# Optimization experiments

Hardware: AMD Instinct MI355X
Metric: run time of the kernel (lower is better)

The kernel has to match this reference:

```python
import jax, jax.numpy as jnp
import numpy as np

# Scalar-only irreps: 8x0e nodes in, 4x0e edge in, 8x0e edge out, 16x0e node out.
N = 50000          # nodes
E = 800000         # edges
MUL_NODE_IN = 8
MUL_EDGE_IN = 4
MUL_Z = 2 * MUL_NODE_IN          # cat([x[i], x[j]]) -> 16
MUL_EDGE_OUT = 8
MUL_NODE_OUT = 16
W_NUMEL = MUL_EDGE_IN * MUL_Z * MUL_EDGE_OUT  # 512 = edge_tp.weight_numel
RAD_IN, RAD_HID = 16, 64         # radial_neurons=[16, 64]


def setup_inputs() -> dict:
    key = jax.random.key(0)
    ks = jax.random.split(key, 7)
    x = jax.random.normal(ks[0], (N, MUL_NODE_IN), dtype=jnp.float32)
    edge_index = jax.random.randint(ks[1], (2, E), 0, N)
    edge_attr = jax.random.normal(ks[2], (E, MUL_EDGE_IN), dtype=jnp.float32)
    edge_len_emb = jax.random.normal(ks[3], (E, RAD_IN), dtype=jnp.float32)
    # radial MLP (e3nn FullyConnectedNet: normalized linear layers, silu)
    w1 = jax.random.normal(ks[4], (RAD_IN, RAD_HID), dtype=jnp.float32)
    w2 = jax.random.normal(ks[5], (RAD_HID, W_NUMEL), dtype=jnp.float32)
    # node_tp internal shared weights: [mul_node_in, mul_edge_out, mul_node_out]
    w_node = jax.random.normal(ks[6], (MUL_NODE_IN, MUL_EDGE_OUT, MUL_NODE_OUT), dtype=jnp.float32)
    return {"x": x, "edge_index": edge_index, "edge_attr": edge_attr,
            "edge_len_emb": edge_len_emb, "w1": w1, "w2": w2, "w_node": w_node}


def reference(x, edge_index, edge_attr, edge_len_emb, w1, w2, w_node):
    i, j = edge_index[0], edge_index[1]
    # radial MLP -> per-edge TP weights (e3nn normalized linears, silu)
    h = jax.nn.silu(edge_len_emb @ w1 / jnp.sqrt(jnp.float32(RAD_IN)))
    w_edge = (h @ w2 / jnp.sqrt(jnp.float32(RAD_HID)))
    w_edge = w_edge.reshape(E, MUL_EDGE_IN, MUL_Z, MUL_EDGE_OUT)
    # gather + concat: z = cat([x[i], x[j]])  [E, 16]
    z = jnp.concatenate([x[i], x[j]], axis=-1)
    # edge_tp: fully-connected scalar TP with path norm 1/sqrt(mul1*mul2)
    edge_out = jnp.einsum('ea,eb,eabk->ek', edge_attr, z, w_edge)
    edge_out = edge_out / jnp.sqrt(jnp.float32(MUL_EDGE_IN * MUL_Z))
    # scatter-sum to destination nodes j
    e_sum = jax.ops.segment_sum(edge_out, j, num_segments=x.shape[0])
    # node_tp: shared internal weights, path norm 1/sqrt(mul1*mul2)
    x_out = jnp.einsum('na,nb,abk->nk', x, e_sum, w_node)
    x_out = x_out / jnp.sqrt(jnp.float32(MUL_NODE_IN * MUL_EDGE_OUT))
    return (x_out, edge_out)
```

## Files before the change

### kernel.cpp

```cpp
#include <hip/hip_runtime.h>


typedef __attribute__((ext_vector_type(8))) short short8;
typedef __attribute__((ext_vector_type(4))) float floatx4;

__device__ inline unsigned short f2bf(float f) {
    union { float f; unsigned u; } v; v.f = f;
    unsigned r = v.u + 0x7FFFu + ((v.u >> 16) & 1u);
    return (unsigned short)(r >> 16);
}

__device__ inline unsigned cvt_pk_bf16(float lo, float hi) {
    unsigned r;
    asm("v_cvt_pk_bf16_f32 %0, %1, %2" : "=v"(r) : "v"(lo), "v"(hi));
    return r;
}

constexpr int TB   = 512;
constexpr int NBLK = 512;

__global__ __launch_bounds__(TB, 2) void edge_kernel(
    const float* __restrict__ x,
    const int*   __restrict__ ei,
    const float* __restrict__ attr,
    const float* __restrict__ emb,
    const float* __restrict__ w1,
    const float* __restrict__ w2,
    float* __restrict__ edge_out,
    float* __restrict__ e_sum,
    int E)
{
    __shared__ __align__(16) unsigned short s_w2t[512 * 64];
    __shared__ __align__(16) float          s_ztA[8 * 16 * 32];

    const int tid  = threadIdx.x;
    const int wave = tid >> 6;
    const int lane = tid & 63;
    const int m16  = lane & 15;
    const int quad = lane >> 4;
    const int par  = m16 >> 3;

    for (int idx = tid; idx < 512 * 64; idx += TB) {
        const int n = idx & 511, k = idx >> 9;
        s_w2t[n * 64 + (k ^ ((n & 7) << 3))] = f2bf(w2[k * 512 + n]);
    }
    __syncthreads();

    short8 w1f[4];
    #pragma unroll
    for (int mt = 0; mt < 4; ++mt) {
        short8 f;
        if (quad < 2) {
            #pragma unroll
            for (int j = 0; j < 8; ++j)
                f[j] = (short)f2bf(w1[(quad * 8 + j) * 64 + mt * 16 + m16]);
        } else {
            #pragma unroll
            for (int j = 0; j < 8; ++j) f[j] = 0;
        }
        w1f[mt] = f;
    }

    float* ztw = s_ztA + wave * 16 * 32;

    const int  wid = blockIdx.x * 8 + wave;
    const int  nw  = NBLK * 8;
    const int  ntiles = E >> 5;
    const bool stg = (quad < 2);
    const int  mst = quad * 16 + m16;

    const int srcA = m16 + 16 * ((2 * quad) & 3);
    const int srcB = m16 + 16 * ((2 * quad + 1) & 3);

    const int swz = (m16 & 7) << 3;
    const int o0  = (quad * 8) ^ swz;
    const int o1  = o0 ^ 32;

    float4 xi0, xi1, xj0, xj1, a4;
    float4 em0a, em0b, em1a, em1b;
    int viN = 0, vjN = 0, vjC = 0;

    if (wid < ntiles && stg) {
        const int e0 = (wid << 5) + mst;
        const int vi = ei[e0];
        vjC = ei[E + e0];
        xi0 = *(const float4*)(x + (size_t)vi * 8);
        xi1 = *(const float4*)(x + (size_t)vi * 8 + 4);
        xj0 = *(const float4*)(x + (size_t)vjC * 8);
        xj1 = *(const float4*)(x + (size_t)vjC * 8 + 4);
        a4  = *(const float4*)(attr + (size_t)e0 * 4);
        const float* ep0 = emb + (size_t)((wid << 5) + m16) * 16 + quad * 8;
        em0a = *(const float4*)ep0;
        em0b = *(const float4*)(ep0 + 4);
        const float* ep1 = emb + (size_t)((wid << 5) + 16 + m16) * 16 + quad * 8;
        em1a = *(const float4*)ep1;
        em1b = *(const float4*)(ep1 + 4);
        const int t1 = (wid + nw < ntiles) ? (wid + nw) : wid;
        const int e1 = (t1 << 5) + mst;
        viN = ei[e1];
        vjN = ei[E + e1];
    }

    for (int tile = wid; tile < ntiles; tile += nw) {
        const int base = tile << 5;

        if (stg) {
            ztw[ 0*32+mst]=xi0.x; ztw[ 1*32+mst]=xi0.y;
            ztw[ 2*32+mst]=xi0.z; ztw[ 3*32+mst]=xi0.w;
            ztw[ 4*32+mst]=xi1.x; ztw[ 5*32+mst]=xi1.y;
            ztw[ 6*32+mst]=xi1.z; ztw[ 7*32+mst]=xi1.w;
            ztw[ 8*32+mst]=xj0.x; ztw[ 9*32+mst]=xj0.y;
            ztw[10*32+mst]=xj0.z; ztw[11*32+mst]=xj0.w;
            ztw[12*32+mst]=xj1.x; ztw[13*32+mst]=xj1.y;
            ztw[14*32+mst]=xj1.z; ztw[15*32+mst]=xj1.w;
        }
        const float4 a4cur = a4;
        const int    vjE   = vjC;

        short8 a1[2];
        {
            union { short8 s8; unsigned u[4]; } uu;
            if (stg) {
                uu.u[0] = cvt_pk_bf16(em0a.x, em0a.y);
                uu.u[1] = cvt_pk_bf16(em0a.z, em0a.w);
                uu.u[2] = cvt_pk_bf16(em0b.x, em0b.y);
                uu.u[3] = cvt_pk_bf16(em0b.z, em0b.w);
            } else {
                uu.u[0]=0u; uu.u[1]=0u; uu.u[2]=0u; uu.u[3]=0u;
            }
            a1[0] = uu.s8;
            if (stg) {
                uu.u[0] = cvt_pk_bf16(em1a.x, em1a.y);
                uu.u[1] = cvt_pk_bf16(em1a.z, em1a.w);
                uu.u[2] = cvt_pk_bf16(em1b.x, em1b.y);
                uu.u[3] = cvt_pk_bf16(em1b.z, em1b.w);
            } else {
                uu.u[0]=0u; uu.u[1]=0u; uu.u[2]=0u; uu.u[3]=0u;
            }
            a1[1] = uu.s8;
        }

        {
            const int tn     = tile + nw;
            const int tn_cl  = (tn  < ntiles) ? tn  : tile;
            const int tnn    = tn + nw;
            const int tnn_cl = (tnn < ntiles) ? tnn : tn_cl;
            if (stg) {
                const int en = (tn_cl << 5) + mst;
                vjC = vjN;
                xi0 = *(const float4*)(x + (size_t)viN * 8);
                xi1 = *(const float4*)(x + (size_t)viN * 8 + 4);
                xj0 = *(const float4*)(x + (size_t)vjN * 8);
                xj1 = *(const float4*)(x + (size_t)vjN * 8 + 4);
                a4  = *(const float4*)(attr + (size_t)en * 4);
                const float* ep0 = emb + (size_t)((tn_cl << 5) + m16) * 16 + quad * 8;
                em0a = *(const float4*)ep0;
                em0b = *(const float4*)(ep0 + 4);
                const float* ep1 = emb + (size_t)((tn_cl << 5) + 16 + m16) * 16 + quad * 8;
                em1a = *(const float4*)ep1;
                em1b = *(const float4*)(ep1 + 4);
                const int enn = (tnn_cl << 5) + mst;
                viN = ei[enn];
                vjN = ei[E + enn];
            }
        }

        short8 a2[2][2];
        #pragma unroll
        for (int s = 0; s < 2; ++s) {
            unsigned p[4][2];
            #pragma unroll
            for (int half = 0; half < 2; ++half) {
                floatx4 c0, c1;
                {
                    floatx4 z4 = {0.f, 0.f, 0.f, 0.f};
                    c0 = __builtin_amdgcn_mfma_f32_16x16x32_bf16(w1f[2*half    ], a1[s], z4, 0, 0, 0);
                    c1 = __builtin_amdgcn_mfma_f32_16x16x32_bf16(w1f[2*half + 1], a1[s], z4, 0, 0, 0);
                }
                #pragma unroll
                for (int h = 0; h < 2; ++h) {
                    const floatx4& c = h ? c1 : c0;
                    float sv[4];
                    #pragma unroll
                    for (int r = 0; r < 4; ++r) {
                        const float u   = c[r] * 0.25f;
                        const float den = 1.f + __expf(-u);
                        sv[r] = u * __builtin_amdgcn_rcpf(den) * 0.015625f;
                    }
                    p[2*half + h][0] = cvt_pk_bf16(sv[0], sv[1]);
                    p[2*half + h][1] = cvt_pk_bf16(sv[2], sv[3]);
                }
            }
            #pragma unroll
            for (int qq = 0; qq < 2; ++qq) {
                union { short8 s8; unsigned u[4]; } uu;
                #pragma unroll
                for (int w = 0; w < 4; ++w) {
                    const int srcLane = (w < 2) ? srcA : srcB;
                    const unsigned vA = (unsigned)__shfl((int)p[2*qq    ][w & 1], srcLane, 64);
                    const unsigned vB = (unsigned)__shfl((int)p[2*qq + 1][w & 1], srcLane, 64);
                    uu.u[w] = (quad & 2) ? vB : vA;
                }
                a2[s][qq] = uu.s8;
            }
        }

        float eacc[2][4];
        #pragma unroll
        for (int s = 0; s < 2; ++s)
            #pragma unroll
            for (int r = 0; r < 4; ++r) eacc[s][r] = 0.f;

        __builtin_amdgcn_s_setprio(1);
        #pragma unroll 1
        for (int g = 0; g < 4; ++g) {
            const float ag = (g == 0) ? a4cur.x : (g == 1) ? a4cur.y
                           : (g == 2) ? a4cur.z : a4cur.w;
            float av[2][4];
            #pragma unroll
            for (int s = 0; s < 2; ++s)
                #pragma unroll
                for (int r = 0; r < 4; ++r)
                    av[s][r] = __shfl(ag, s * 16 + quad * 4 + r, 64);

            float tacc[2][4];
            #pragma unroll
            for (int s = 0; s < 2; ++s)
                #pragma unroll
                for (int r = 0; r < 4; ++r) tacc[s][r] = 0.f;

            #pragma unroll
            for (int tt = 0; tt < 8; ++tt) {
                const int t = g * 8 + tt;
                const unsigned short* wrow = s_w2t + (16 * t + m16) * 64;
                short8 b2[2];
                b2[0] = *(const short8*)(wrow + o0);
                b2[1] = *(const short8*)(wrow + o1);
                const int b_idx = (2 * tt + par) & 15;
                #pragma unroll
                for (int s = 0; s < 2; ++s) {
                    floatx4 c = {0.f, 0.f, 0.f, 0.f};
                    c = __builtin_amdgcn_mfma_f32_16x16x32_bf16(a2[s][0], b2[0], c, 0, 0, 0);
                    c = __builtin_amdgcn_mfma_f32_16x16x32_bf16(a2[s][1], b2[1], c, 0, 0, 0);
                    const float4 zv = *(const float4*)(ztw + b_idx * 32 + s * 16 + quad * 4);
                    tacc[s][0] = fmaf(c[0], zv.x, tacc[s][0]);
                    tacc[s][1] = fmaf(c[1], zv.y, tacc[s][1]);
                    tacc[s][2] = fmaf(c[2], zv.z, tacc[s][2]);
                    tacc[s][3] = fmaf(c[3], zv.w, tacc[s][3]);
                }
            }
            #pragma unroll
            for (int s = 0; s < 2; ++s)
                #pragma unroll
                for (int r = 0; r < 4; ++r)
                    eacc[s][r] = fmaf(av[s][r], tacc[s][r], eacc[s][r]);
        }
        __builtin_amdgcn_s_setprio(0);

        #pragma unroll
        for (int s = 0; s < 2; ++s)
            #pragma unroll
            for (int r = 0; r < 4; ++r)
                eacc[s][r] += __shfl_xor(eacc[s][r], 8, 64);

        int vjr[2][4];
        #pragma unroll
        for (int s = 0; s < 2; ++s)
            #pragma unroll
            for (int r = 0; r < 4; ++r)
                vjr[s][r] = __shfl(vjE, s * 16 + quad * 4 + r, 64);

        if (m16 < 8) {
            #pragma unroll
            for (int s = 0; s < 2; ++s) {
                #pragma unroll
                for (int r = 0; r < 4; ++r) {
                    const int e = base + s * 16 + quad * 4 + r;
                    edge_out[(size_t)e * 8 + m16] = eacc[s][r];
                    atomicAdd(e_sum + (size_t)vjr[s][r] * 8 + m16, eacc[s][r]);
                }
            }
        }
    }
}

__global__ __launch_bounds__(256) void node_kernel(
    const float* __restrict__ x,
    const float* __restrict__ e_sum,
    const float* __restrict__ w_node,
    float* __restrict__ x_out,
    int N)
{
    __shared__ float s_w[8 * 8 * 16];
    for (int idx = threadIdx.x; idx < 1024; idx += 256) s_w[idx] = w_node[idx];
    __syncthreads();

    const int n = blockIdx.x * 256 + threadIdx.x;
    if (n >= N) return;

    float xa[8], eb[8];
    #pragma unroll
    for (int a = 0; a < 8; ++a) xa[a] = x[(size_t)n * 8 + a];
    #pragma unroll
    for (int b = 0; b < 8; ++b) eb[b] = e_sum[(size_t)n * 8 + b];

    float out[16];
    #pragma unroll
    for (int k = 0; k < 16; ++k) out[k] = 0.f;

    const float4* wv = (const float4*)s_w;
    #pragma unroll
    for (int a = 0; a < 8; ++a) {
        #pragma unroll
        for (int b = 0; b < 8; ++b) {
            const float t = xa[a] * eb[b] * 0.125f;
            #pragma unroll
            for (int k4 = 0; k4 < 4; ++k4) {
                const float4 w = wv[(a * 8 + b) * 4 + k4];
                out[k4 * 4 + 0] = fmaf(t, w.x, out[k4 * 4 + 0]);
                out[k4 * 4 + 1] = fmaf(t, w.y, out[k4 * 4 + 1]);
                out[k4 * 4 + 2] = fmaf(t, w.z, out[k4 * 4 + 2]);
                out[k4 * 4 + 3] = fmaf(t, w.w, out[k4 * 4 + 3]);
            }
        }
    }

    float4* xo = (float4*)(x_out + (size_t)n * 16);
    #pragma unroll
    for (int k4 = 0; k4 < 4; ++k4)
        xo[k4] = make_float4(out[k4 * 4 + 0], out[k4 * 4 + 1],
                             out[k4 * 4 + 2], out[k4 * 4 + 3]);
}

extern "C" void kernel_launch(void* const* d_in, const int* in_sizes, int n_in,
                              void* d_out, int out_size, void* d_ws, size_t ws_size,
                              hipStream_t stream) {
    const float* x      = (const float*)d_in[0];
    const int*   ei     = (const int*)d_in[1];
    const float* attr   = (const float*)d_in[2];
    const float* emb    = (const float*)d_in[3];
    const float* w1     = (const float*)d_in[4];
    const float* w2     = (const float*)d_in[5];
    const float* w_node = (const float*)d_in[6];

    const int N = in_sizes[0] / 8;
    const int E = in_sizes[2] / 4;

    float* x_out    = (float*)d_out;
    float* edge_out = (float*)d_out + (size_t)N * 16;
    float* e_sum    = (float*)d_ws;

    hipMemsetAsync(e_sum, 0, (size_t)N * 8 * sizeof(float), stream);

    edge_kernel<<<NBLK, TB, 0, stream>>>(x, ei, attr, emb, w1, w2,
                                         edge_out, e_sum, E);

    node_kernel<<<(N + 255) / 256, 256, 0, stream>>>(x, e_sum, w_node, x_out, N);
}
```

Measured before the change: 205.7 us.

## Use 1024-thread blocks and stage edge attrs and dst indices in LDS

Doubles the block size to 1024 threads with half as many blocks, so one copy of the 64 KB bf16 w2 table in LDS serves 16 waves instead of 8. It also replaces the per-group cross-lane shuffles of edge attributes and destination indices with writes to per-wave LDS buffers that are read back as float4 and int4. This trades shuffle work and repeated w2 staging for extra LDS traffic and a larger LDS footprint, and launch bounds of 1024 may cap registers per thread and cause spills.

```diff
diff --git a/kernel.cpp b/kernel.cpp
--- a/kernel.cpp
+++ b/kernel.cpp
@@ -16,10 +16,13 @@
     return r;
 }
 
-constexpr int TB   = 512;
-constexpr int NBLK = 512;
-
-__global__ __launch_bounds__(TB, 2) void edge_kernel(
+constexpr int TB    = 1024;
+constexpr int NBLK  = 256;
+constexpr int NWAVE = TB / 64;
+
+constexpr int AT_LDF = 32;
+
+__global__ __launch_bounds__(TB) void edge_kernel(
     const float* __restrict__ x,
     const int*   __restrict__ ei,
     const float* __restrict__ attr,
@@ -31,7 +34,9 @@
     int E)
 {
     __shared__ __align__(16) unsigned short s_w2t[512 * 64];
-    __shared__ __align__(16) float          s_ztA[8 * 16 * 32];
+    __shared__ __align__(16) float          s_ztA[NWAVE * 16 * 32];
+    __shared__ __align__(16) float          s_atA[NWAVE * 4 * AT_LDF];
+    __shared__ int                          s_vjA[NWAVE * 32];
 
     const int tid  = threadIdx.x;
     const int wave = tid >> 6;
@@ -62,9 +67,11 @@
     }
 
     float* ztw = s_ztA + wave * 16 * 32;
-
-    const int  wid = blockIdx.x * 8 + wave;
-    const int  nw  = NBLK * 8;
+    float* atw = s_atA + wave * 4 * AT_LDF;
+    int*   vjw = s_vjA + wave * 32;
+
+    const int  wid = blockIdx.x * NWAVE + wave;
+    const int  nw  = NBLK * NWAVE;
     const int  ntiles = E >> 5;
     const bool stg = (quad < 2);
     const int  mst = quad * 16 + m16;
@@ -113,9 +120,10 @@
             ztw[10*32+mst]=xj0.z; ztw[11*32+mst]=xj0.w;
             ztw[12*32+mst]=xj1.x; ztw[13*32+mst]=xj1.y;
             ztw[14*32+mst]=xj1.z; ztw[15*32+mst]=xj1.w;
-        }
-        const float4 a4cur = a4;
-        const int    vjE   = vjC;
+            atw[0*AT_LDF+mst]=a4.x;   atw[1*AT_LDF+mst]=a4.y;
+            atw[2*AT_LDF+mst]=a4.z;   atw[3*AT_LDF+mst]=a4.w;
+            vjw[mst] = vjC;
+        }
 
         short8 a1[2];
         {
@@ -214,14 +222,13 @@
         __builtin_amdgcn_s_setprio(1);
         #pragma unroll 1
         for (int g = 0; g < 4; ++g) {
-            const float ag = (g == 0) ? a4cur.x : (g == 1) ? a4cur.y
-                           : (g == 2) ? a4cur.z : a4cur.w;
             float av[2][4];
             #pragma unroll
-            for (int s = 0; s < 2; ++s)
-                #pragma unroll
-                for (int r = 0; r < 4; ++r)
-                    av[s][r] = __shfl(ag, s * 16 + quad * 4 + r, 64);
+            for (int s = 0; s < 2; ++s) {
+                const float4 a4v = *(const float4*)(atw + g * AT_LDF + s * 16 + quad * 4);
+                av[s][0] = a4v.x; av[s][1] = a4v.y;
+                av[s][2] = a4v.z; av[s][3] = a4v.w;
+            }
 
             float tacc[2][4];
             #pragma unroll
@@ -263,21 +270,16 @@
             for (int r = 0; r < 4; ++r)
                 eacc[s][r] += __shfl_xor(eacc[s][r], 8, 64);
 
-        int vjr[2][4];
-        #pragma unroll
-        for (int s = 0; s < 2; ++s)
-            #pragma unroll
-            for (int r = 0; r < 4; ++r)
-                vjr[s][r] = __shfl(vjE, s * 16 + quad * 4 + r, 64);
-
         if (m16 < 8) {
             #pragma unroll
             for (int s = 0; s < 2; ++s) {
+                const int4 vjq = *(const int4*)(vjw + s * 16 + quad * 4);
+                const int vjr[4] = {vjq.x, vjq.y, vjq.z, vjq.w};
                 #pragma unroll
                 for (int r = 0; r < 4; ++r) {
                     const int e = base + s * 16 + quad * 4 + r;
                     edge_out[(size_t)e * 8 + m16] = eacc[s][r];
-                    atomicAdd(e_sum + (size_t)vjr[s][r] * 8 + m16, eacc[s][r]);
+                    atomicAdd(e_sum + (size_t)vjr[r] * 8 + m16, eacc[s][r]);
                 }
             }
         }
```

Result: slower. 463.1 us (+125.1%).
